# Kernel optimization log

Hardware: AMD Instinct MI355X
Metric: run time of the kernel (lower is better)

## Reference

```python
import jax, jax.numpy as jnp
import numpy as np

N, E, G = 50000, 600000, 512   # nodes, edges, graphs
F, D, L = 128, 128, 3          # in_features, hidden dim, num_gc_layers
ED = D * L                      # embedding_dim (readout='concat')
C = 1.0                         # curvature
MIN_NORM = 1e-15
BALL_EPS = 4e-3                 # hgcn PoincareBall proj eps for float32


def _logmap0(p, c):
    sc = jnp.sqrt(c)
    n = jnp.clip(jnp.linalg.norm(p, axis=-1, keepdims=True), MIN_NORM, None)
    return p / (sc * n) * jnp.arctanh(jnp.clip(sc * n, -1 + 1e-15, 1 - 1e-15))


def _expmap0(u, c):
    sc = jnp.sqrt(c)
    n = jnp.clip(jnp.linalg.norm(u, axis=-1, keepdims=True), MIN_NORM, None)
    return jnp.tanh(sc * n) * u / (sc * n)


def _proj(x, c):
    n = jnp.clip(jnp.linalg.norm(x, axis=-1, keepdims=True), MIN_NORM, None)
    maxn = (1.0 - BALL_EPS) / jnp.sqrt(c)
    return jnp.where(n > maxn, x / n * maxn, x)


def _gcn(x, W, b, src, dst):
    h = x @ W
    deg = jax.ops.segment_sum(jnp.ones_like(dst, dtype=h.dtype), dst, num_segments=N) + 1.0
    dinv = deg ** -0.5
    msg = h[src] * (dinv[src] * dinv[dst])[:, None]           # [E, D]
    agg = jax.ops.segment_sum(msg, dst, num_segments=N) + h * (dinv * dinv)[:, None]
    return agg + b


def _encoder(x, Ws, bs, src, dst, batch):
    xs = []
    for W, b in zip(Ws, bs):
        x = jax.nn.relu(_gcn(x, W, b, src, dst))
        xs.append(x)
    # readout='concat' with global_add_pool
    g = jnp.concatenate([jax.ops.segment_sum(h, batch, num_segments=G) for h in xs], axis=1)
    return g, jnp.concatenate(xs, axis=1)


def _mlp(x, W1, W2):  # proj_head: Linear (no bias), ReLU, Linear (no bias)
    return jax.nn.relu(x @ W1) @ W2


def setup_inputs() -> dict:
    key = jax.random.key(0)
    ks = jax.random.split(key, 24)

    def xav(k, i, o):
        return jax.random.normal(k, (i, o), dtype=jnp.float32) * np.float32(np.sqrt(2.0 / (i + o)))

    inp = {
        'x':   jax.random.normal(ks[0], (N, F), dtype=jnp.float32) * 1e-3,  # points inside the ball
        'x_s': jax.random.normal(ks[1], (N, F), dtype=jnp.float32) * 1e-3,
        'src': jax.random.randint(ks[2], (E,), 0, N, dtype=jnp.int32),
        'dst': jax.random.randint(ks[3], (E,), 0, N, dtype=jnp.int32),
        'batch': jnp.sort(jax.random.randint(ks[4], (N,), 0, G, dtype=jnp.int32)),
        # feature-branch GCN encoder
        'Wf0': xav(ks[5], F, D), 'Wf1': xav(ks[6], D, D), 'Wf2': xav(ks[7], D, D),
        'bf0': jnp.zeros((D,), jnp.float32), 'bf1': jnp.zeros((D,), jnp.float32), 'bf2': jnp.zeros((D,), jnp.float32),
        # structure-branch GCN encoder
        'Ws0': xav(ks[8], F, D), 'Ws1': xav(ks[9], D, D), 'Ws2': xav(ks[10], D, D),
        'bs0': jnp.zeros((D,), jnp.float32), 'bs1': jnp.zeros((D,), jnp.float32), 'bs2': jnp.zeros((D,), jnp.float32),
        # proj heads (biases removed by init_emb)
        'P1': xav(ks[11], ED, ED), 'P2': xav(ks[12], ED, ED),
        'G1': xav(ks[13], 2 * ED, ED), 'G2': xav(ks[14], ED, ED),
    }
    return inp


def reference(x, x_s, Wf0, Wf1, Wf2, bf0, bf1, bf2, Ws0, Ws1, Ws2, bs0, bs1, bs2, P1, P2, G1, G2, src, dst, batch):
    xt_f = _logmap0(x, C)
    xt_s = _logmap0(x_s, C)
    g_f, n_f = _encoder(xt_f, (Wf0, Wf1, Wf2), (bf0, bf1, bf2), src, dst, batch)
    g_s, n_s = _encoder(xt_s, (Ws0, Ws1, Ws2), (bs0, bs1, bs2), src, dst, batch)
    g = _mlp(jnp.concatenate((g_f, g_s), axis=1), G1, G2)
    e = lambda t: _proj(_expmap0(t, C), C)
    return (e(g), e(_mlp(g_f, P1, P2)), e(_mlp(n_f, P1, P2)), e(_mlp(g_s, P1, P2)), e(_mlp(n_s, P1, P2)))
```

## Files before the change

kernel.cpp:

```cpp
#include <hip/hip_runtime.h>
#include <math.h>

#define N_NODES 50000
#define N_EDGES 600000
#define N_GRAPHS 512
#define F_IN 128
#define D_HID 128
#define EDIM 384
#define M_ALL (N_NODES + N_GRAPHS)

typedef __attribute__((ext_vector_type(8))) short bf16x8;
typedef __attribute__((ext_vector_type(4))) float f32x4;

static __device__ __forceinline__ float wave_reduce_sum(float s) {
#pragma unroll
  for (int off = 32; off > 0; off >>= 1) s += __shfl_xor(s, off, 64);
  return s;
}

static __device__ __forceinline__ int wave_reduce_sum_i(int s) {
#pragma unroll
  for (int off = 32; off > 0; off >>= 1) s += __shfl_xor(s, off, 64);
  return s;
}

static __device__ __forceinline__ short f2b(float f) {
  unsigned u = __float_as_uint(f);
  unsigned r = (u + 0x7FFFu + ((u >> 16) & 1u)) >> 16;
  return (short)r;
}

static __device__ __forceinline__ float b2f(short s) {
  return __uint_as_float(((unsigned)(unsigned short)s) << 16);
}


#define SCAN_BS 256
#define SCAN_NB ((N_NODES + SCAN_BS - 1) / SCAN_BS)

__global__ __launch_bounds__(SCAN_BS) void init_kernel(const int* __restrict__ batch,
                                                       int* __restrict__ cnt,
                                                       int* __restrict__ gptr) {
  int i = blockIdx.x * SCAN_BS + threadIdx.x;
  if (i < N_NODES) cnt[i] = 0;
  if (i <= N_GRAPHS) {
    int lo = 0, hi = N_NODES;
    while (lo < hi) { int mid = (lo + hi) >> 1; if (batch[mid] < i) lo = mid + 1; else hi = mid; }
    gptr[i] = lo;
  }
}

__global__ void hist_kernel(const int* __restrict__ dst, int* __restrict__ cnt) {
  int i = blockIdx.x * blockDim.x + threadIdx.x;
  if (i < N_EDGES) atomicAdd(&cnt[dst[i]], 1);
}

__global__ __launch_bounds__(SCAN_BS) void scan1_kernel(const int* __restrict__ cnt,
                                                        int* __restrict__ row_ptr,
                                                        int* __restrict__ bsum) {
  __shared__ int wsum[4];
  int tid = threadIdx.x, lane = tid & 63, wid = tid >> 6;
  int idx = blockIdx.x * SCAN_BS + tid;
  int v = (idx < N_NODES) ? cnt[idx] : 0;
  int x = v;
#pragma unroll
  for (int off = 1; off < 64; off <<= 1) {
    int t = __shfl_up(x, off, 64);
    if (lane >= off) x += t;
  }
  if (lane == 63) wsum[wid] = x;
  __syncthreads();
  int pre = 0, tot = 0;
#pragma unroll
  for (int w = 0; w < 4; ++w) { int s = wsum[w]; tot += s; if (w < wid) pre += s; }
  if (idx < N_NODES) row_ptr[idx + 1] = x + pre;
  if (tid == 0) bsum[blockIdx.x] = tot;
}

__global__ __launch_bounds__(SCAN_BS) void scan3_kernel(const int* __restrict__ cnt,
                                                        const int* __restrict__ bsum,
                                                        int* __restrict__ row_ptr,
                                                        int* __restrict__ cursor,
                                                        float* __restrict__ dinv) {
  __shared__ int ws[4];
  int tid = threadIdx.x, lane = tid & 63, wid = tid >> 6;
  int v = 0;
  if (tid < SCAN_NB && tid < blockIdx.x) v = bsum[tid];
  v = wave_reduce_sum_i(v);
  if (lane == 0) ws[wid] = v;
  __syncthreads();
  int boff = ws[0] + ws[1] + ws[2] + ws[3];
  int idx = blockIdx.x * SCAN_BS + tid;
  if (idx >= N_NODES) return;
  int val = row_ptr[idx + 1] + boff;
  row_ptr[idx + 1] = val;
  int c = cnt[idx];
  cursor[idx] = val - c;
  dinv[idx] = 1.0f / sqrtf((float)(c + 1));
  if (idx == 0) row_ptr[0] = 0;
}

__global__ void scatter_kernel(const int* __restrict__ src, const int* __restrict__ dst,
                               const float* __restrict__ dinv, int* __restrict__ cursor,
                               int* __restrict__ col, float* __restrict__ ew) {
  int e = blockIdx.x * blockDim.x + threadIdx.x;
  if (e >= N_EDGES) return;
  int s = src[e], d = dst[e];
  int pos = atomicAdd(&cursor[d], 1);
  col[pos] = s;
  ew[pos] = dinv[s] * dinv[d];
}


struct WcSeg { const float* W; short* Wt; int K; int Nc; };
struct WcArgs { WcSeg seg[10]; };

__global__ void wconv_all_kernel(WcArgs a) {
  int sidx = blockIdx.y;
  WcSeg s = a.seg[sidx];
  int i = blockIdx.x * blockDim.x + threadIdx.x;
  if (i >= s.K * s.Nc) return;
  int k = i / s.Nc, n = i - k * s.Nc;
  s.Wt[(size_t)n * s.K + k] = f2b(s.W[i]);
}


__global__ __launch_bounds__(256) void logmap2_kernel(const float* __restrict__ x,
                                                      const float* __restrict__ x_s,
                                                      short* __restrict__ Ab) {
  int w = blockIdx.x * 4 + (threadIdx.x >> 6);
  int lane = threadIdx.x & 63;
  if (w >= 2 * N_NODES) return;
  int br = (w >= N_NODES) ? 1 : 0;
  int row = br ? (w - N_NODES) : w;
  const float* xr = (br ? x_s : x) + (size_t)row * F_IN;
  float2 v = *(const float2*)(xr + lane * 2);
  float s = wave_reduce_sum(v.x * v.x + v.y * v.y);
  float n = sqrtf(s);
  float nc = fmaxf(n, 1e-15f);
  float f = atanhf(fminf(nc, 0.9999999f)) / nc;
  short2 o; o.x = f2b(v.x * f); o.y = f2b(v.y * f);
  *(short2*)(Ab + (size_t)row * 256 + br * 128 + lane * 2) = o;
}


__global__ __launch_bounds__(256) void agg2_kernel(const short* __restrict__ Xin, int lda,
                                                   const float* __restrict__ dinv,
                                                   const int* __restrict__ row_ptr,
                                                   const int* __restrict__ col,
                                                   const float* __restrict__ ew,
                                                   short* __restrict__ Xa) {
  int node = blockIdx.x * 4 + (threadIdx.x >> 6);
  int lane = threadIdx.x & 63;
  if (node >= N_NODES) return;
  float di = dinv[node];
  float wsf = di * di;
  short4 sv = *(const short4*)(Xin + (size_t)node * lda + lane * 4);
  float a0 = b2f(sv.x) * wsf, a1 = b2f(sv.y) * wsf, a2 = b2f(sv.z) * wsf, a3 = b2f(sv.w) * wsf;
  int s = row_ptr[node], e = row_ptr[node + 1];
  int j = s;
  for (; j + 4 <= e; j += 4) {
    int c0 = col[j], c1 = col[j + 1], c2 = col[j + 2], c3 = col[j + 3];
    float w0 = ew[j], w1 = ew[j + 1], w2 = ew[j + 2], w3 = ew[j + 3];
    short4 v0 = *(const short4*)(Xin + (size_t)c0 * lda + lane * 4);
    short4 v1 = *(const short4*)(Xin + (size_t)c1 * lda + lane * 4);
    short4 v2 = *(const short4*)(Xin + (size_t)c2 * lda + lane * 4);
    short4 v3 = *(const short4*)(Xin + (size_t)c3 * lda + lane * 4);
    a0 += b2f(v0.x) * w0; a1 += b2f(v0.y) * w0; a2 += b2f(v0.z) * w0; a3 += b2f(v0.w) * w0;
    a0 += b2f(v1.x) * w1; a1 += b2f(v1.y) * w1; a2 += b2f(v1.z) * w1; a3 += b2f(v1.w) * w1;
    a0 += b2f(v2.x) * w2; a1 += b2f(v2.y) * w2; a2 += b2f(v2.z) * w2; a3 += b2f(v2.w) * w2;
    a0 += b2f(v3.x) * w3; a1 += b2f(v3.y) * w3; a2 += b2f(v3.z) * w3; a3 += b2f(v3.w) * w3;
  }
  for (; j < e; ++j) {
    float w0 = ew[j];
    short4 v0 = *(const short4*)(Xin + (size_t)col[j] * lda + lane * 4);
    a0 += b2f(v0.x) * w0; a1 += b2f(v0.y) * w0; a2 += b2f(v0.z) * w0; a3 += b2f(v0.w) * w0;
  }
  short4 o; o.x = f2b(a0); o.y = f2b(a1); o.z = f2b(a2); o.w = f2b(a3);
  *(short4*)(Xa + (size_t)node * 256 + lane * 4) = o;
}


#define LDK 40

struct GemmZArgs {
  const short* A[2];
  const short* Bt[2];
  const float* bias[2];
  short* Cb[2];
  float* Cf[2];
  float* Cf2[2];
  int lda, ldc, M, Nc, K, kexp, do_relu, split;
};

__global__ __launch_bounds__(256) void mfma_gemmz_kernel(GemmZArgs g) {
  __shared__ __align__(16) short As[128 * LDK];
  __shared__ __align__(16) short Bs[128 * LDK];
  int z = blockIdx.z;
  const short* __restrict__ A = g.A[z];
  const short* __restrict__ Bt = g.Bt[z];
  int tid = threadIdx.x;
  int wave = tid >> 6, lane = tid & 63;
  int wr = (wave >> 1) * 64, wc = (wave & 1) * 64;
  int q = lane >> 4, m = lane & 15;
  int row0 = blockIdx.x * 128, col0 = blockIdx.y * 128;
  f32x4 acc[4][4] = {};
  for (int k0 = 0; k0 < g.K; k0 += 32) {
#pragma unroll
    for (int p = 0; p < 2; ++p) {
      int idx = p * 256 + tid;
      int r = idx >> 2, kc = (idx & 3) * 8;
      int gr = row0 + r;
      int kk = k0 + kc;
      int acol = g.kexp ? (kk + ((kk >> 7) << 7)) : kk;
      float4 v = make_float4(0.f, 0.f, 0.f, 0.f);
      if (gr < g.M) v = *(const float4*)(A + (size_t)gr * g.lda + acol);
      *(float4*)(As + r * LDK + kc) = v;
      float4 w = *(const float4*)(Bt + (size_t)(col0 + r) * g.K + kk);
      *(float4*)(Bs + r * LDK + kc) = w;
    }
    __syncthreads();
    bf16x8 af[4], bfr[4];
#pragma unroll
    for (int i = 0; i < 4; ++i) {
      af[i]  = *(const bf16x8*)(As + (wr + i * 16 + m) * LDK + q * 8);
      bfr[i] = *(const bf16x8*)(Bs + (wc + i * 16 + m) * LDK + q * 8);
    }
#pragma unroll
    for (int i = 0; i < 4; ++i)
#pragma unroll
      for (int j = 0; j < 4; ++j)
        acc[i][j] = __builtin_amdgcn_mfma_f32_16x16x32_bf16(af[i], bfr[j], acc[i][j], 0, 0, 0);
    __syncthreads();
  }
  const float* __restrict__ bias = g.bias[z];
  short* __restrict__ Cb = g.Cb[z];
  float* __restrict__ Cf = g.Cf[z];
  float* __restrict__ Cf2 = g.Cf2[z];
#pragma unroll
  for (int i = 0; i < 4; ++i) {
#pragma unroll
    for (int r = 0; r < 4; ++r) {
      int rr = row0 + wr + i * 16 + q * 4 + r;
      if (rr >= g.M) continue;
#pragma unroll
      for (int j = 0; j < 4; ++j) {
        int cc = col0 + wc + j * 16 + m;
        float v = acc[i][j][r];
        if (bias) v += bias[cc];
        if (g.do_relu) v = fmaxf(v, 0.0f);
        if (Cb) Cb[(size_t)rr * g.ldc + cc] = f2b(v);
        else if (rr < g.split) Cf[(size_t)rr * g.Nc + cc] = v;
        else Cf2[(size_t)(rr - g.split) * g.Nc + cc] = v;
      }
    }
  }
}


__global__ __launch_bounds__(768) void pool2_kernel(const short* __restrict__ NB,
                                                    const int* __restrict__ gptr,
                                                    short* __restrict__ GCb,
                                                    short* __restrict__ nbappend) {
  int g = blockIdx.x, t = threadIdx.x;
  int s = gptr[g], e = gptr[g + 1];
  float acc = 0.0f;
  for (int i = s; i < e; ++i) acc += b2f(NB[(size_t)i * 768 + t]);
  short bv = f2b(acc);
  int l = t >> 8, rem = t & 255, b = rem >> 7, c = rem & 127;
  GCb[(size_t)g * 768 + b * 384 + l * 128 + c] = bv;
  nbappend[(size_t)g * 768 + t] = bv;
}


__global__ __launch_bounds__(256) void exp_proj_kernel(float* __restrict__ y, int nrows) {
  int row = blockIdx.x * 4 + (threadIdx.x >> 6);
  int lane = threadIdx.x & 63;
  if (row >= nrows) return;
  float* p = y + (size_t)row * EDIM;
  float v[6];
  float s = 0.0f;
#pragma unroll
  for (int j = 0; j < 6; ++j) { v[j] = p[lane + j * 64]; s += v[j] * v[j]; }
  s = wave_reduce_sum(s);
  float n = fmaxf(sqrtf(s), 1e-15f);
  float th = tanhf(n);
  float f = th / n;
  float n2 = fmaxf(th, 1e-15f);
  const float maxn = 1.0f - 4e-3f;
  if (n2 > maxn) f *= maxn / n2;
#pragma unroll
  for (int j = 0; j < 6; ++j) p[lane + j * 64] = v[j] * f;
}


extern "C" void kernel_launch(void* const* d_in, const int* in_sizes, int n_in,
                              void* d_out, int out_size, void* d_ws, size_t ws_size,
                              hipStream_t stream) {
  (void)in_sizes; (void)n_in; (void)out_size; (void)ws_size;
  const float* x   = (const float*)d_in[0];
  const float* x_s = (const float*)d_in[1];
  const int* src   = (const int*)d_in[2];
  const int* dst   = (const int*)d_in[3];
  const int* batch = (const int*)d_in[4];
  const float* Wf[3] = {(const float*)d_in[5], (const float*)d_in[6], (const float*)d_in[7]};
  const float* bf[3] = {(const float*)d_in[8], (const float*)d_in[9], (const float*)d_in[10]};
  const float* Wsb[3] = {(const float*)d_in[11], (const float*)d_in[12], (const float*)d_in[13]};
  const float* bs[3] = {(const float*)d_in[14], (const float*)d_in[15], (const float*)d_in[16]};
  const float* P1 = (const float*)d_in[17];
  const float* P2 = (const float*)d_in[18];
  const float* G1 = (const float*)d_in[19];
  const float* G2 = (const float*)d_in[20];
  float* out = (float*)d_out;

  char* w = (char*)d_ws;
  auto alloc = [&](size_t bytes) {
    char* p = w;
    w += (bytes + 255) & ~(size_t)255;
    return p;
  };
  short* HIDb2 = (short*)alloc((size_t)2 * M_ALL * 384 * 2);
  short* Ab    = HIDb2;
  short* Xa    = (short*)alloc((size_t)N_NODES * 256 * 2);
  short* NB    = (short*)alloc((size_t)M_ALL * 768 * 2);
  int* cnt     = (int*)alloc((size_t)N_NODES * 4);
  int* row_ptr = (int*)alloc((size_t)(N_NODES + 1) * 4);
  int* cursor  = (int*)alloc((size_t)N_NODES * 4);
  float* dinv  = (float*)alloc((size_t)N_NODES * 4);
  int* col     = (int*)alloc((size_t)N_EDGES * 4);
  float* ew    = (float*)alloc((size_t)N_EDGES * 4);
  int* gptr    = (int*)alloc((size_t)(N_GRAPHS + 1) * 4);
  int* bsum    = (int*)alloc(256 * 4);
  short* GCb   = (short*)alloc((size_t)N_GRAPHS * 768 * 2);
  short* GHb   = (short*)alloc((size_t)N_GRAPHS * 384 * 2);
  short* P1t   = (short*)alloc((size_t)EDIM * EDIM * 2);
  short* P2t   = (short*)alloc((size_t)EDIM * EDIM * 2);
  short* G1t   = (short*)alloc((size_t)768 * EDIM * 2);
  short* G2t   = (short*)alloc((size_t)EDIM * EDIM * 2);
  short* Wft[3], *Wst[3];
  for (int l = 0; l < 3; ++l) {
    Wft[l] = (short*)alloc((size_t)128 * 128 * 2);
    Wst[l] = (short*)alloc((size_t)128 * 128 * 2);
  }

  {
    WcArgs wa;
    wa.seg[0] = {P1, P1t, EDIM, EDIM};
    wa.seg[1] = {P2, P2t, EDIM, EDIM};
    wa.seg[2] = {G1, G1t, 768, EDIM};
    wa.seg[3] = {G2, G2t, EDIM, EDIM};
    for (int l = 0; l < 3; ++l) {
      wa.seg[4 + l] = {Wf[l], Wft[l], 128, 128};
      wa.seg[7 + l] = {Wsb[l], Wst[l], 128, 128};
    }
    wconv_all_kernel<<<dim3((768 * EDIM + 255) / 256, 10), 256, 0, stream>>>(wa);
  }

  init_kernel<<<SCAN_NB, SCAN_BS, 0, stream>>>(batch, cnt, gptr);
  hist_kernel<<<(N_EDGES + 255) / 256, 256, 0, stream>>>(dst, cnt);
  scan1_kernel<<<SCAN_NB, SCAN_BS, 0, stream>>>(cnt, row_ptr, bsum);
  scan3_kernel<<<SCAN_NB, SCAN_BS, 0, stream>>>(cnt, bsum, row_ptr, cursor, dinv);
  scatter_kernel<<<(N_EDGES + 255) / 256, 256, 0, stream>>>(src, dst, dinv, cursor, col, ew);

  const size_t OUT0 = 0;
  const size_t OUT1 = (size_t)N_GRAPHS * EDIM;
  const size_t OUT2 = OUT1 + (size_t)N_GRAPHS * EDIM;
  const size_t OUT3 = OUT2 + (size_t)N_NODES * EDIM;

  const int gx_layer = (N_NODES + 127) / 128;
  const int gx_mfma  = (M_ALL + 127) / 128;
  const int gx_agg   = (N_NODES + 3) / 4;

  logmap2_kernel<<<(2 * N_NODES + 3) / 4, 256, 0, stream>>>(x, x_s, Ab);

  const short* cur = Ab;
  int clda = 256;
  for (int l = 0; l < 3; ++l) {
    agg2_kernel<<<gx_agg, 256, 0, stream>>>(cur, clda, dinv, row_ptr, col, ew, Xa);
    GemmZArgs ga = {};
    ga.A[0] = Xa;        ga.A[1] = Xa + 128;
    ga.Bt[0] = Wft[l];   ga.Bt[1] = Wst[l];
    ga.bias[0] = bf[l];  ga.bias[1] = bs[l];
    ga.Cb[0] = NB + l * 256;        ga.Cb[1] = NB + l * 256 + 128;
    ga.lda = 256; ga.ldc = 768; ga.M = N_NODES; ga.Nc = 128; ga.K = 128;
    ga.kexp = 0; ga.do_relu = 1; ga.split = 0;
    mfma_gemmz_kernel<<<dim3(gx_layer, 1, 2), 256, 0, stream>>>(ga);
    cur = NB + l * 256;
    clda = 768;
  }

  pool2_kernel<<<N_GRAPHS, 768, 0, stream>>>(NB, gptr, GCb, NB + (size_t)N_NODES * 768);

  const int gx_g = (N_GRAPHS + 127) / 128;
  {
    GemmZArgs g1 = {};
    g1.A[0] = g1.A[1] = GCb;
    g1.Bt[0] = g1.Bt[1] = G1t;
    g1.Cb[0] = g1.Cb[1] = GHb;
    g1.lda = 768; g1.ldc = 384; g1.M = N_GRAPHS; g1.Nc = EDIM; g1.K = 768;
    g1.kexp = 0; g1.do_relu = 1; g1.split = 0;
    mfma_gemmz_kernel<<<dim3(gx_g, 3, 1), 256, 0, stream>>>(g1);

    GemmZArgs g2 = {};
    g2.A[0] = g2.A[1] = GHb;
    g2.Bt[0] = g2.Bt[1] = G2t;
    g2.Cf[0] = g2.Cf[1] = out + OUT0;
    g2.Cf2[0] = g2.Cf2[1] = out + OUT0;
    g2.lda = 384; g2.ldc = 0; g2.M = N_GRAPHS; g2.Nc = EDIM; g2.K = EDIM;
    g2.kexp = 0; g2.do_relu = 0; g2.split = 1 << 30;
    mfma_gemmz_kernel<<<dim3(gx_g, 3, 1), 256, 0, stream>>>(g2);
  }

  float* ghead_out[2] = {out + OUT1, out + OUT3};
  float* node_out[2]  = {out + OUT2, out + OUT3 + (size_t)N_GRAPHS * EDIM};
  {
    GemmZArgs h1 = {};
    h1.A[0] = NB;                 h1.A[1] = NB + 128;
    h1.Bt[0] = h1.Bt[1] = P1t;
    h1.Cb[0] = HIDb2;             h1.Cb[1] = HIDb2 + (size_t)M_ALL * 384;
    h1.lda = 768; h1.ldc = 384; h1.M = M_ALL; h1.Nc = EDIM; h1.K = EDIM;
    h1.kexp = 1; h1.do_relu = 1; h1.split = 0;
    mfma_gemmz_kernel<<<dim3(gx_mfma, 3, 2), 256, 0, stream>>>(h1);

    GemmZArgs h2 = {};
    h2.A[0] = HIDb2;              h2.A[1] = HIDb2 + (size_t)M_ALL * 384;
    h2.Bt[0] = h2.Bt[1] = P2t;
    h2.Cf[0] = node_out[0];       h2.Cf[1] = node_out[1];
    h2.Cf2[0] = ghead_out[0];     h2.Cf2[1] = ghead_out[1];
    h2.lda = 384; h2.ldc = 0; h2.M = M_ALL; h2.Nc = EDIM; h2.K = EDIM;
    h2.kexp = 0; h2.do_relu = 0; h2.split = N_NODES;
    mfma_gemmz_kernel<<<dim3(gx_mfma, 3, 2), 256, 0, stream>>>(h2);
  }

  const int nrows_exp = N_GRAPHS + 2 * M_ALL;
  exp_proj_kernel<<<(nrows_exp + 3) / 4, 256, 0, stream>>>(out + OUT0, nrows_exp);
}
```

Baseline: 844.8 us.

## Fuse second projection GEMM with expmap/proj row normalization in full-width head kernel

Adds a head2 kernel in which each block computes all 384 output columns for 128 rows. It can then take the row norm in registers and apply the expmap0 and ball projection before writing fp32 output. This removes the separate exp_proj pass, which re-read and re-wrote roughly 100k×384 floats. In exchange each thread holds 24 accumulators, the block uses a larger B tile in shared memory, and fewer blocks are launched along the column dimension, which may lower occupancy.

```diff
diff --git a/kernel.cpp b/kernel.cpp
--- a/kernel.cpp
+++ b/kernel.cpp
@@ -188,9 +188,7 @@
   const short* Bt[2];
   const float* bias[2];
   short* Cb[2];
-  float* Cf[2];
-  float* Cf2[2];
-  int lda, ldc, M, Nc, K, kexp, do_relu, split;
+  int lda, ldc, M, Nc, K, kexp, do_relu;
 };
 
 __global__ __launch_bounds__(256) void mfma_gemmz_kernel(GemmZArgs g) {
@@ -235,8 +233,6 @@
   }
   const float* __restrict__ bias = g.bias[z];
   short* __restrict__ Cb = g.Cb[z];
-  float* __restrict__ Cf = g.Cf[z];
-  float* __restrict__ Cf2 = g.Cf2[z];
 #pragma unroll
   for (int i = 0; i < 4; ++i) {
 #pragma unroll
@@ -249,10 +245,81 @@
         float v = acc[i][j][r];
         if (bias) v += bias[cc];
         if (g.do_relu) v = fmaxf(v, 0.0f);
-        if (Cb) Cb[(size_t)rr * g.ldc + cc] = f2b(v);
-        else if (rr < g.split) Cf[(size_t)rr * g.Nc + cc] = v;
-        else Cf2[(size_t)(rr - g.split) * g.Nc + cc] = v;
+        Cb[(size_t)rr * g.ldc + cc] = f2b(v);
       }
+    }
+  }
+}
+
+
+struct Head2Args {
+  const short* A[2];
+  const short* Bt2;
+  float* Cf[2];
+  float* Cf2[2];
+  int lda, M, split;
+};
+
+__global__ __launch_bounds__(512) void head2_kernel(Head2Args g) {
+  __shared__ __align__(16) short As[128 * LDK];
+  __shared__ __align__(16) short Bs[384 * LDK];
+  int z = blockIdx.z;
+  const short* __restrict__ A = g.A[z];
+  const short* __restrict__ Bt = g.Bt2;
+  int tid = threadIdx.x;
+  int wave = tid >> 6, lane = tid & 63;
+  int q = lane >> 4, m = lane & 15;
+  int row0 = blockIdx.x * 128;
+  f32x4 acc[24] = {};
+  for (int k0 = 0; k0 < 384; k0 += 32) {
+    {
+      int r = tid >> 2, kc = (tid & 3) * 8;
+      int gr = row0 + r;
+      float4 v = make_float4(0.f, 0.f, 0.f, 0.f);
+      if (gr < g.M) v = *(const float4*)(A + (size_t)gr * g.lda + k0 + kc);
+      *(float4*)(As + r * LDK + kc) = v;
+    }
+#pragma unroll
+    for (int p = 0; p < 3; ++p) {
+      int idx = p * 512 + tid;
+      int r = idx >> 2, kc = (idx & 3) * 8;
+      float4 w0 = *(const float4*)(Bt + (size_t)r * 384 + k0 + kc);
+      *(float4*)(Bs + r * LDK + kc) = w0;
+    }
+    __syncthreads();
+    bf16x8 af = *(const bf16x8*)(As + (wave * 16 + m) * LDK + q * 8);
+#pragma unroll
+    for (int j = 0; j < 24; ++j) {
+      bf16x8 bfr = *(const bf16x8*)(Bs + (j * 16 + m) * LDK + q * 8);
+      acc[j] = __builtin_amdgcn_mfma_f32_16x16x32_bf16(af, bfr, acc[j], 0, 0, 0);
+    }
+    __syncthreads();
+  }
+  float* __restrict__ Cf = g.Cf[z];
+  float* __restrict__ Cf2 = g.Cf2[z];
+  const float maxn = 1.0f - 4e-3f;
+#pragma unroll
+  for (int r = 0; r < 4; ++r) {
+    float s = 0.0f;
+#pragma unroll
+    for (int j = 0; j < 24; ++j) s += acc[j][r] * acc[j][r];
+    s += __shfl_xor(s, 1, 64);
+    s += __shfl_xor(s, 2, 64);
+    s += __shfl_xor(s, 4, 64);
+    s += __shfl_xor(s, 8, 64);
+    int rr = row0 + wave * 16 + q * 4 + r;
+    if (rr >= g.M) continue;
+    float n = fmaxf(sqrtf(s), 1e-15f);
+    float th = tanhf(n);
+    float f = th / n;
+    float n2 = fmaxf(th, 1e-15f);
+    if (n2 > maxn) f *= maxn / n2;
+    if (rr < g.split) {
+#pragma unroll
+      for (int j = 0; j < 24; ++j) Cf[(size_t)rr * 384 + j * 16 + m] = acc[j][r] * f;
+    } else {
+#pragma unroll
+      for (int j = 0; j < 24; ++j) Cf2[(size_t)(rr - g.split) * 384 + j * 16 + m] = acc[j][r] * f;
     }
   }
 }
@@ -270,27 +337,6 @@
   int l = t >> 8, rem = t & 255, b = rem >> 7, c = rem & 127;
   GCb[(size_t)g * 768 + b * 384 + l * 128 + c] = bv;
   nbappend[(size_t)g * 768 + t] = bv;
-}
-
-
-__global__ __launch_bounds__(256) void exp_proj_kernel(float* __restrict__ y, int nrows) {
-  int row = blockIdx.x * 4 + (threadIdx.x >> 6);
-  int lane = threadIdx.x & 63;
-  if (row >= nrows) return;
-  float* p = y + (size_t)row * EDIM;
-  float v[6];
-  float s = 0.0f;
-#pragma unroll
-  for (int j = 0; j < 6; ++j) { v[j] = p[lane + j * 64]; s += v[j] * v[j]; }
-  s = wave_reduce_sum(s);
-  float n = fmaxf(sqrtf(s), 1e-15f);
-  float th = tanhf(n);
-  float f = th / n;
-  float n2 = fmaxf(th, 1e-15f);
-  const float maxn = 1.0f - 4e-3f;
-  if (n2 > maxn) f *= maxn / n2;
-#pragma unroll
-  for (int j = 0; j < 6; ++j) p[lane + j * 64] = v[j] * f;
 }
 
 
@@ -383,7 +429,7 @@
     ga.bias[0] = bf[l];  ga.bias[1] = bs[l];
     ga.Cb[0] = NB + l * 256;        ga.Cb[1] = NB + l * 256 + 128;
     ga.lda = 256; ga.ldc = 768; ga.M = N_NODES; ga.Nc = 128; ga.K = 128;
-    ga.kexp = 0; ga.do_relu = 1; ga.split = 0;
+    ga.kexp = 0; ga.do_relu = 1;
     mfma_gemmz_kernel<<<dim3(gx_layer, 1, 2), 256, 0, stream>>>(ga);
     cur = NB + l * 256;
     clda = 768;
@@ -398,17 +444,16 @@
     g1.Bt[0] = g1.Bt[1] = G1t;
     g1.Cb[0] = g1.Cb[1] = GHb;
     g1.lda = 768; g1.ldc = 384; g1.M = N_GRAPHS; g1.Nc = EDIM; g1.K = 768;
-    g1.kexp = 0; g1.do_relu = 1; g1.split = 0;
+    g1.kexp = 0; g1.do_relu = 1;
     mfma_gemmz_kernel<<<dim3(gx_g, 3, 1), 256, 0, stream>>>(g1);
 
-    GemmZArgs g2 = {};
+    Head2Args g2 = {};
     g2.A[0] = g2.A[1] = GHb;
-    g2.Bt[0] = g2.Bt[1] = G2t;
+    g2.Bt2 = G2t;
     g2.Cf[0] = g2.Cf[1] = out + OUT0;
     g2.Cf2[0] = g2.Cf2[1] = out + OUT0;
-    g2.lda = 384; g2.ldc = 0; g2.M = N_GRAPHS; g2.Nc = EDIM; g2.K = EDIM;
-    g2.kexp = 0; g2.do_relu = 0; g2.split = 1 << 30;
-    mfma_gemmz_kernel<<<dim3(gx_g, 3, 1), 256, 0, stream>>>(g2);
+    g2.lda = 384; g2.M = N_GRAPHS; g2.split = 1 << 30;
+    head2_kernel<<<dim3(gx_g, 1, 1), 512, 0, stream>>>(g2);
   }
 
   float* ghead_out[2] = {out + OUT1, out + OUT3};
@@ -419,19 +464,15 @@
     h1.Bt[0] = h1.Bt[1] = P1t;
     h1.Cb[0] = HIDb2;             h1.Cb[1] = HIDb2 + (size_t)M_ALL * 384;
     h1.lda = 768; h1.ldc = 384; h1.M = M_ALL; h1.Nc = EDIM; h1.K = EDIM;
-    h1.kexp = 1; h1.do_relu = 1; h1.split = 0;
+    h1.kexp = 1; h1.do_relu = 1;
     mfma_gemmz_kernel<<<dim3(gx_mfma, 3, 2), 256, 0, stream>>>(h1);
 
-    GemmZArgs h2 = {};
+    Head2Args h2 = {};
     h2.A[0] = HIDb2;              h2.A[1] = HIDb2 + (size_t)M_ALL * 384;
-    h2.Bt[0] = h2.Bt[1] = P2t;
+    h2.Bt2 = P2t;
     h2.Cf[0] = node_out[0];       h2.Cf[1] = node_out[1];
     h2.Cf2[0] = ghead_out[0];     h2.Cf2[1] = ghead_out[1];
-    h2.lda = 384; h2.ldc = 0; h2.M = M_ALL; h2.Nc = EDIM; h2.K = EDIM;
-    h2.kexp = 0; h2.do_relu = 0; h2.split = N_NODES;
-    mfma_gemmz_kernel<<<dim3(gx_mfma, 3, 2), 256, 0, stream>>>(h2);
-  }
-
-  const int nrows_exp = N_GRAPHS + 2 * M_ALL;
-  exp_proj_kernel<<<(nrows_exp + 3) / 4, 256, 0, stream>>>(out + OUT0, nrows_exp);
-}
+    h2.lda = 384; h2.M = M_ALL; h2.split = N_NODES;
+    head2_kernel<<<dim3(gx_mfma, 1, 2), 512, 0, stream>>>(h2);
+  }
+}
```

Result: faster. 770.5 us (-8.8%).
